# Optimization experiments

Hardware: AMD Instinct MI355X
Metric: run time of the kernel (lower is better)

## Reference

```python
import jax, jax.numpy as jnp
import numpy as np

H = 12  # num_attention_heads


def setup_inputs() -> dict:
    key = jax.random.key(0)
    ks = jax.random.split(key, 7)
    B, T, L, D = 4, 64, 128, 768
    input_ids = jax.random.randint(ks[0], (B, T, L), 0, 30000, dtype=jnp.int32)
    speaker_ids = jax.random.randint(ks[1], (B, T), 0, 8, dtype=jnp.int32)
    token_embeddings = jax.random.normal(ks[2], (B, T, L, D), dtype=jnp.float32)
    edu_embeddings = jax.random.normal(ks[3], (B, T, D), dtype=jnp.float32)
    s = 1.0 / np.sqrt(D)
    Wk = jax.random.normal(ks[4], (D, D), dtype=jnp.float32) * s
    Wv = jax.random.normal(ks[5], (D, D), dtype=jnp.float32) * s
    Wq = jax.random.normal(ks[6], (D, D), dtype=jnp.float32) * s
    return {"input_ids": input_ids, "speaker_ids": speaker_ids,
            "token_embeddings": token_embeddings, "edu_embeddings": edu_embeddings,
            "Wk": Wk, "Wv": Wv, "Wq": Wq}


def reference(input_ids, speaker_ids, token_embeddings, edu_embeddings, Wk, Wv, Wq):
    B, T, L = input_ids.shape
    D = token_embeddings.shape[-1]
    d = D // H
    # per-turn keys/values, split into heads: [B,T,H,d]
    k = (edu_embeddings @ Wk.T).reshape(B, T, H, d)
    v = (edu_embeddings @ Wv.T).reshape(B, T, H, d)
    # per-head outer products k (x) v: [B,T,H,d,d]
    kv = jnp.einsum('bthd,bthe->bthde', k, v)
    # speaker-segmented inclusive prefix sum: M[b,t] = sum_{u<=t, spk[u]==spk[t]} kv[b,u]
    same = speaker_ids[:, None, :] == speaker_ids[:, :, None]        # [B,T(t),T(u)]
    causal = jnp.tril(jnp.ones((T, T), dtype=bool))                  # u <= t (inclusive)
    A = (same & causal).astype(kv.dtype)                             # [B,T,T]
    M = jnp.einsum('btu,buhde->bthde', A, kv)                        # [B,T,H,d,d]
    # token queries attend into their turn's speaker memory matrix
    q = (token_embeddings @ Wq.T).reshape(B, T, L, H, d)
    a = jnp.einsum('btlhd,bthde->btlhe', q, M).reshape(B, T, L, D)
    return token_embeddings + a
```

## Files before the change

kernel.cpp:

```cpp
#include <hip/hip_runtime.h>
#include <hip/hip_bf16.h>

#define NB 4
#define NT 64
#define NL 128
#define ND 768
#define NH 12
#define HD 64

typedef __attribute__((ext_vector_type(8))) short short8;
typedef __attribute__((ext_vector_type(4))) float f32x4;

typedef __attribute__((address_space(3))) unsigned int lds_u32;
typedef __attribute__((address_space(1))) const unsigned int glob_u32;

static __device__ __forceinline__ unsigned short f2b(float x) {
    __hip_bfloat16 h = __float2bfloat16(x);
    return *reinterpret_cast<unsigned short*>(&h);
}
static __device__ __forceinline__ void gl2lds16(const void* g, void* l) {
    __builtin_amdgcn_global_load_lds((glob_u32*)g, (lds_u32*)l, 16, 0, 0);
}

#define WQ_C   73728u
#define EDU_C  98304u
#define WK_C   172032u
#define NCHUNK 245760u

__global__ __launch_bounds__(256) void conv_bf16(
    const float* __restrict__ Wq, const float* __restrict__ edu,
    const float* __restrict__ Wk, const float* __restrict__ Wv,
    unsigned short* __restrict__ dst)
{
    size_t c = (size_t)blockIdx.x * 256 + threadIdx.x;
    if (c >= NCHUNK) return;
    const float* s;
    if (c < WQ_C)       s = Wq  + c * 8;
    else if (c < EDU_C) s = edu + (c - WQ_C)  * 8;
    else if (c < WK_C)  s = Wk  + (c - EDU_C) * 8;
    else                s = Wv  + (c - WK_C)  * 8;
    float4 x = *(const float4*)s;
    float4 y = *(const float4*)(s + 4);
    unsigned short v[8];
    v[0] = f2b(x.x); v[1] = f2b(x.y); v[2] = f2b(x.z); v[3] = f2b(x.w);
    v[4] = f2b(y.x); v[5] = f2b(y.y); v[6] = f2b(y.z); v[7] = f2b(y.w);
    *(short8*)(dst + c * 8) = *(short8*)v;
}

__global__ __launch_bounds__(256) void kvm(
    const unsigned short* __restrict__ edu_b,
    const unsigned short* __restrict__ wk_b,
    const unsigned short* __restrict__ wv_b,
    const int* __restrict__ spk,
    unsigned short* __restrict__ Mt)
{
    const int h = blockIdx.x, b = blockIdx.y, eh = blockIdx.z;

    __shared__ float bucket[8][32][65];
    __shared__ float k_s[64][68];
    __shared__ float v_s[64][36];
    __shared__ __align__(16) unsigned short stage[10240];
    __shared__ int spk_s[64];
    unsigned short* edu_s = stage;
    unsigned short* wk_s  = stage + 4096;
    unsigned short* wv_s  = stage + 8192;

    const int tid = threadIdx.x, lane = tid & 63, wvx = tid >> 6;
    const int lr = lane & 15, lg = lane >> 4, r8 = lane >> 3, l8 = lane & 7;

    { float* p = &bucket[0][0][0];
      for (int i = tid; i < 8 * 32 * 65; i += 256) p[i] = 0.f; }
    if (tid < 64) spk_s[tid] = spk[b * NT + tid];

    const unsigned short* edub = edu_b + (size_t)(b * 64) * ND;
    const unsigned short* wkb  = wk_b + (size_t)(h * 64) * ND;
    const unsigned short* wvb  = wv_b + (size_t)(h * 64 + eh * 32) * ND;

    f32x4 acc_k[4], acc_v[2];
    #pragma unroll
    for (int i = 0; i < 4; i++) acc_k[i] = (f32x4){0.f, 0.f, 0.f, 0.f};
    #pragma unroll
    for (int i = 0; i < 2; i++) acc_v[i] = (f32x4){0.f, 0.f, 0.f, 0.f};

    const int sswz = ((l8 ^ r8) * 8);

    for (int k0 = 0; k0 < ND; k0 += 64) {
        __syncthreads();
        #pragma unroll
        for (int j = 0; j < 5; j++) {
            const int cid = wvx * 5 + j;
            const unsigned short* gs; unsigned short* ls;
            if (cid < 8)       { gs = edub + (size_t)(cid * 8 + r8) * ND;        ls = edu_s + cid * 512; }
            else if (cid < 16) { gs = wkb  + (size_t)((cid - 8) * 8 + r8) * ND;  ls = wk_s + (cid - 8) * 512; }
            else               { gs = wvb  + (size_t)((cid - 16) * 8 + r8) * ND; ls = wv_s + (cid - 16) * 512; }
            gl2lds16(gs + k0 + sswz, ls);
        }
        __syncthreads();
        #pragma unroll
        for (int k32 = 0; k32 < 2; k32++) {
            const int cx = (((k32 * 4 + lg) ^ (lr & 7)) * 8);
            short8 eb = *(const short8*)&edu_s[(wvx * 16 + lr) * 64 + cx];
            #pragma unroll
            for (int jb = 0; jb < 4; jb++) {
                short8 ak = *(const short8*)&wk_s[(jb * 16 + lr) * 64 + cx];
                acc_k[jb] = __builtin_amdgcn_mfma_f32_16x16x32_bf16(ak, eb, acc_k[jb], 0, 0, 0);
            }
            #pragma unroll
            for (int jb = 0; jb < 2; jb++) {
                short8 av = *(const short8*)&wv_s[(jb * 16 + lr) * 64 + cx];
                acc_v[jb] = __builtin_amdgcn_mfma_f32_16x16x32_bf16(av, eb, acc_v[jb], 0, 0, 0);
            }
        }
    }

    {
        const int t = wvx * 16 + lr;
        #pragma unroll
        for (int jb = 0; jb < 4; jb++) *(f32x4*)&k_s[t][jb * 16 + lg * 4] = acc_k[jb];
        #pragma unroll
        for (int jb = 0; jb < 2; jb++) *(f32x4*)&v_s[t][jb * 16 + lg * 4] = acc_v[jb];
    }
    __syncthreads();

    const int e = tid & 31, dg = tid >> 5;
    for (int t = 0; t < NT; t++) {
        const int s = spk_s[t];
        const float vv = v_s[t][e];
        unsigned short tmp[8];
        #pragma unroll
        for (int jj = 0; jj < 8; jj++) {
            float m = bucket[s][e][dg * 8 + jj] + k_s[t][dg * 8 + jj] * vv;
            bucket[s][e][dg * 8 + jj] = m;
            tmp[jj] = f2b(m);
        }
        unsigned short* mpp = Mt + (((size_t)(b * NT + t) * NH + h) * HD + eh * 32 + e) * HD + dg * 8;
        *(short8*)mpp = *(short8*)tmp;
    }
}

__global__ __launch_bounds__(256, 2) void fused_qm(
    const float* __restrict__ te,
    const unsigned short* __restrict__ wq_b,
    const unsigned short* __restrict__ Mt,
    float* __restrict__ out)
{
    const int orig = blockIdx.x;
    const int id   = (orig & 7) * 192 + (orig >> 3);
    const int hp   = id % 6;
    const int bt   = id / 6;

    __shared__ __align__(16) unsigned short smem[32768];
    unsigned short* te0 = smem;
    unsigned short* te1 = smem + 8192;
    unsigned short* wq0 = smem + 16384;
    unsigned short* wq1 = smem + 24576;
    unsigned short* q_s = smem;

    const int tid  = threadIdx.x;
    const int lane = tid & 63;
    const int wvx  = tid >> 6;
    const int lr   = lane & 15;
    const int lg   = lane >> 4;
    const int wm   = wvx >> 1;
    const int wn   = wvx & 1;
    const int r8   = lane >> 3;
    const int l8   = lane & 7;
    const int sswz = (l8 ^ r8) * 8;
    const int srow = tid >> 3;
    const int sc   = tid & 7;

    const float*          teb = te + (size_t)bt * NL * ND;
    const unsigned short* wqb = wq_b + (size_t)hp * 128 * ND;

    f32x4 acc[4][4];
    #pragma unroll
    for (int i = 0; i < 4; i++)
        #pragma unroll
        for (int j = 0; j < 4; j++) acc[i][j] = (f32x4){0.f, 0.f, 0.f, 0.f};

    float4 ldA[4][2], ldB[4][2];

    auto LOADREG = [&](float4 (&dst)[4][2], int k0) {
        #pragma unroll
        for (int p = 0; p < 4; p++) {
            const int r    = p * 32 + srow;
            const int clog = sc ^ (srow & 7);
            const float* g = teb + (size_t)r * ND + k0 + clog * 8;
            dst[p][0] = *(const float4*)g;
            dst[p][1] = *(const float4*)(g + 4);
        }
    };
    auto CVTWRITE = [&](unsigned short* tebuf, const float4 (&src)[4][2]) {
        #pragma unroll
        for (int p = 0; p < 4; p++) {
            const int r = p * 32 + srow;
            unsigned short v[8];
            v[0] = f2b(src[p][0].x); v[1] = f2b(src[p][0].y);
            v[2] = f2b(src[p][0].z); v[3] = f2b(src[p][0].w);
            v[4] = f2b(src[p][1].x); v[5] = f2b(src[p][1].y);
            v[6] = f2b(src[p][1].z); v[7] = f2b(src[p][1].w);
            *(short8*)&tebuf[r * 64 + sc * 8] = *(short8*)v;
        }
    };
    auto WQSTAGE = [&](unsigned short* buf, int k0) {
        #pragma unroll
        for (int j = 0; j < 4; j++) {
            const int rbase = wvx * 32 + j * 8;
            gl2lds16(wqb + (size_t)(rbase + r8) * ND + k0 + sswz, buf + rbase * 64);
        }
    };
    auto COMPUTE = [&](const unsigned short* tes, const unsigned short* wqs) {
        #pragma unroll
        for (int k32 = 0; k32 < 2; k32++) {
            const int cx = (((k32 * 4 + lg) ^ (lr & 7)) * 8);
            short8 af[4], bfv[4];
            #pragma unroll
            for (int tm = 0; tm < 4; tm++)
                af[tm] = *(const short8*)&wqs[(wm * 64 + tm * 16 + lr) * 64 + cx];
            #pragma unroll
            for (int tn = 0; tn < 4; tn++)
                bfv[tn] = *(const short8*)&tes[(wn * 64 + tn * 16 + lr) * 64 + cx];
            #pragma unroll
            for (int tm = 0; tm < 4; tm++)
                #pragma unroll
                for (int tn = 0; tn < 4; tn++)
                    acc[tm][tn] = __builtin_amdgcn_mfma_f32_16x16x32_bf16(
                        af[tm], bfv[tn], acc[tm][tn], 0, 0, 0);
        }
    };

    LOADREG(ldA, 0);
    LOADREG(ldB, 64);
    WQSTAGE(wq0, 0);
    CVTWRITE(te0, ldA);
    __syncthreads();

    for (int kt = 0; kt < 12; kt += 2) {
        if (kt + 2 < 12) LOADREG(ldA, (kt + 2) * 64);
        WQSTAGE(wq1, (kt + 1) * 64);
        CVTWRITE(te1, ldB);
        COMPUTE(te0, wq0);
        __syncthreads();
        if (kt + 3 < 12) LOADREG(ldB, (kt + 3) * 64);
        if (kt + 2 < 12) { WQSTAGE(wq0, (kt + 2) * 64); CVTWRITE(te0, ldA); }
        COMPUTE(te1, wq1);
        __syncthreads();
    }

    #pragma unroll
    for (int tm = 0; tm < 4; tm++) {
        const int d0 = wm * 64 + tm * 16 + lg * 4;
        #pragma unroll
        for (int tn = 0; tn < 4; tn++) {
            const int ltok = wn * 64 + tn * 16 + lr;
            f32x4 a = acc[tm][tn];
            uint2 w2;
            w2.x = (unsigned)f2b(a.x) | ((unsigned)f2b(a.y) << 16);
            w2.y = (unsigned)f2b(a.z) | ((unsigned)f2b(a.w) << 16);
            *(uint2*)&q_s[ltok * 136 + d0] = w2;
        }
    }

    const int h2 = wvx & 1;
    const int lh = wvx >> 1;
    const unsigned short* mp = Mt + ((size_t)(bt * NH) + hp * 2 + h2) * (HD * HD);
    short8 bfr[8];
    #pragma unroll
    for (int tn = 0; tn < 4; tn++)
        #pragma unroll
        for (int k32 = 0; k32 < 2; k32++)
            bfr[tn * 2 + k32] =
                *(const short8*)&mp[(tn * 16 + lr) * 64 + k32 * 32 + lg * 8];
    __syncthreads();

    f32x4 acc2[4][4];
    #pragma unroll
    for (int i = 0; i < 4; i++)
        #pragma unroll
        for (int j = 0; j < 4; j++) acc2[i][j] = (f32x4){0.f, 0.f, 0.f, 0.f};

    #pragma unroll
    for (int k32 = 0; k32 < 2; k32++) {
        const int ko = k32 * 32 + lg * 8;
        short8 af[4];
        #pragma unroll
        for (int tm = 0; tm < 4; tm++)
            af[tm] = *(const short8*)&q_s[(lh * 64 + tm * 16 + lr) * 136 + h2 * 64 + ko];
        #pragma unroll
        for (int tm = 0; tm < 4; tm++)
            #pragma unroll
            for (int tn = 0; tn < 4; tn++)
                acc2[tm][tn] = __builtin_amdgcn_mfma_f32_16x16x32_bf16(
                    af[tm], bfr[tn * 2 + k32], acc2[tm][tn], 0, 0, 0);
    }

    float* ob = out + (size_t)bt * NL * ND;
    #pragma unroll
    for (int tm = 0; tm < 4; tm++) {
        const int l0 = lh * 64 + tm * 16 + lg * 4;
        #pragma unroll
        for (int tn = 0; tn < 4; tn++) {
            const int cg = hp * 128 + h2 * 64 + tn * 16 + lr;
            f32x4 a = acc2[tm][tn];
            #pragma unroll
            for (int r = 0; r < 4; r++) {
                size_t gi = (size_t)(l0 + r) * ND + cg;
                ob[gi] = teb[gi] + a[r];
            }
        }
    }
}

extern "C" void kernel_launch(void* const* d_in, const int* in_sizes, int n_in,
                              void* d_out, int out_size, void* d_ws, size_t ws_size,
                              hipStream_t stream)
{
    const int*   spk = (const int*)d_in[1];
    const float* te  = (const float*)d_in[2];
    const float* edu = (const float*)d_in[3];
    const float* Wk  = (const float*)d_in[4];
    const float* Wv  = (const float*)d_in[5];
    const float* Wq  = (const float*)d_in[6];
    float* out = (float*)d_out;

    unsigned short* bf    = (unsigned short*)d_ws;
    unsigned short* wq_bb = bf;
    unsigned short* edu_b = bf + 589824u;
    unsigned short* wk_bb = bf + 786432u;
    unsigned short* wv_bb = bf + 1376256u;
    unsigned short* Mtbuf = bf + 1966080u;

    conv_bf16<<<960,             256, 0, stream>>>(Wq, edu, Wk, Wv, bf);
    kvm      <<<dim3(NH, NB, 2), 256, 0, stream>>>(edu_b, wk_bb, wv_bb, spk, Mtbuf);
    fused_qm <<<6 * NT * NB,     256, 0, stream>>>(te, wq_bb, Mtbuf, out);
}
```

Measured before the change: 107.3 us.

## Replace syncthreads with fine-grained vmcnt waits in Q-projection pipeline

Rewrites the double-buffered Q projection main loop as a fully unrolled single-step loop. __syncthreads is replaced with explicit s_waitcnt vmcnt counts plus raw s_barrier, so outstanding global loads (register prefetch and LDS-direct Wq stages) can stay in flight across iterations instead of being drained at every barrier. It also hoists the swizzle column computation. The hand-counted vmcnt values must match the exact number of issued loads, or the race risk is silent corruption.

```diff
diff --git a/kernel.cpp b/kernel.cpp
--- a/kernel.cpp
+++ b/kernel.cpp
@@ -168,6 +168,7 @@
     const int sswz = (l8 ^ r8) * 8;
     const int srow = tid >> 3;
     const int sc   = tid & 7;
+    const int clog = sc ^ (srow & 7);
 
     const float*          teb = te + (size_t)bt * NL * ND;
     const unsigned short* wqb = wq_b + (size_t)hp * 128 * ND;
@@ -183,9 +184,7 @@
     auto LOADREG = [&](float4 (&dst)[4][2], int k0) {
         #pragma unroll
         for (int p = 0; p < 4; p++) {
-            const int r    = p * 32 + srow;
-            const int clog = sc ^ (srow & 7);
-            const float* g = teb + (size_t)r * ND + k0 + clog * 8;
+            const float* g = teb + (size_t)(p * 32 + srow) * ND + k0 + clog * 8;
             dst[p][0] = *(const float4*)g;
             dst[p][1] = *(const float4*)(g + 4);
         }
@@ -232,19 +231,31 @@
     LOADREG(ldA, 0);
     LOADREG(ldB, 64);
     WQSTAGE(wq0, 0);
+    asm volatile("s_waitcnt vmcnt(12)" ::: "memory");
+    __builtin_amdgcn_sched_barrier(0);
     CVTWRITE(te0, ldA);
-    __syncthreads();
-
-    for (int kt = 0; kt < 12; kt += 2) {
-        if (kt + 2 < 12) LOADREG(ldA, (kt + 2) * 64);
-        WQSTAGE(wq1, (kt + 1) * 64);
-        CVTWRITE(te1, ldB);
-        COMPUTE(te0, wq0);
-        __syncthreads();
-        if (kt + 3 < 12) LOADREG(ldB, (kt + 3) * 64);
-        if (kt + 2 < 12) { WQSTAGE(wq0, (kt + 2) * 64); CVTWRITE(te0, ldA); }
-        COMPUTE(te1, wq1);
-        __syncthreads();
+    asm volatile("s_waitcnt lgkmcnt(0)" ::: "memory");
+    __builtin_amdgcn_s_barrier();
+
+    #pragma unroll
+    for (int kt = 0; kt < 12; ++kt) {
+        const int cur = kt & 1;
+        if (kt + 2 < 12) {
+            if (cur == 0) LOADREG(ldA, (kt + 2) * 64);
+            else          LOADREG(ldB, (kt + 2) * 64);
+        }
+        if (kt + 1 < 12) WQSTAGE(cur == 0 ? wq1 : wq0, (kt + 1) * 64);
+        if (kt <= 9)       { asm volatile("s_waitcnt vmcnt(12)" ::: "memory"); }
+        else if (kt == 10) { asm volatile("s_waitcnt vmcnt(4)"  ::: "memory"); }
+        else               { asm volatile("s_waitcnt vmcnt(0)"  ::: "memory"); }
+        __builtin_amdgcn_sched_barrier(0);
+        __builtin_amdgcn_s_barrier();
+        if (kt + 1 < 12)
+            CVTWRITE(cur == 0 ? te1 : te0, cur == 0 ? ldB : ldA);
+        COMPUTE(cur == 0 ? te0 : te1, cur == 0 ? wq0 : wq1);
+        asm volatile("s_waitcnt lgkmcnt(0)" ::: "memory");
+        __builtin_amdgcn_sched_barrier(0);
+        __builtin_amdgcn_s_barrier();
     }
 
     #pragma unroll
```

New measurement: 113.5 us. 1.06x slower.
